# Performance work log

Hardware: AMD Instinct MI355X
Metric: run time of the kernel (lower is better)

Reference implementation:

```python
import jax, jax.numpy as jnp
import numpy as np

N_DIM = 32
N_HEADS = 4
HEAD_SIZE = N_DIM // N_HEADS  # 8


def setup_inputs() -> dict:
    key = jax.random.key(0)
    ks = jax.random.split(key, 9)
    B, T = 16, 2048
    s = 1.0 / np.sqrt(N_DIM)
    inp = {
        "x": jax.random.normal(ks[0], (B, T, N_DIM), dtype=jnp.float32),
        "Wq": jax.random.uniform(ks[1], (N_DIM, N_DIM), jnp.float32, -s, s),
        "bq": jax.random.uniform(ks[2], (N_DIM,), jnp.float32, -s, s),
        "Wk": jax.random.uniform(ks[3], (N_DIM, N_DIM), jnp.float32, -s, s),
        "bk": jax.random.uniform(ks[4], (N_DIM,), jnp.float32, -s, s),
        "Wv": jax.random.uniform(ks[5], (N_DIM, N_DIM), jnp.float32, -s, s),
        "bv": jax.random.uniform(ks[6], (N_DIM,), jnp.float32, -s, s),
        "Wp": jax.random.uniform(ks[7], (N_DIM, N_DIM), jnp.float32, -s, s),
        "bp": jax.random.uniform(ks[8], (N_DIM,), jnp.float32, -s, s),
    }
    return inp


def reference(x, Wq, bq, Wk, bk, Wv, bv, Wp, bp):
    b, t, c = x.shape
    # nn.Linear: y = x @ W^T + b
    def heads(W, bias):
        y = jnp.einsum("btc,dc->btd", x, W) + bias
        return y.reshape(b, t, N_HEADS, HEAD_SIZE).transpose(0, 2, 1, 3)  # [b,h,t,d]

    q = heads(Wq, bq)
    k = heads(Wk, bk)
    v = heads(Wv, bv)

    scores = jnp.einsum("bhqd,bhkd->bhqk", q, k) / np.sqrt(HEAD_SIZE)  # [b,h,t,t]
    causal = jnp.tril(jnp.ones((t, t), dtype=bool))
    scores = jnp.where(causal[None, None], scores, -jnp.inf)
    weights = jax.nn.softmax(scores, axis=-1)
    # dropout layers are identity in eval mode
    z = jnp.einsum("bhqk,bhkd->bhqd", weights, v)
    z = z.transpose(0, 2, 1, 3).reshape(b, t, N_DIM)
    z = jnp.einsum("btc,dc->btd", z, Wp) + bp
    return z
```

## Files before the change

### kernel.cpp

```cpp
#include <hip/hip_runtime.h>
#include <math.h>

#define BB 16
#define TT 2048
#define CC 32
#define HH 4
#define DD 8

#define KBS 2056
#define VRS 264
#define VBS (9 * VRS)
#define ZP 33

typedef __fp16 h2  __attribute__((ext_vector_type(2)));
typedef __fp16 h8  __attribute__((ext_vector_type(8)));
typedef float  fx16 __attribute__((ext_vector_type(16)));
typedef int    i4v __attribute__((ext_vector_type(4)));

__device__ __forceinline__ h2 pkh(float a, float b) {
#if __has_builtin(__builtin_amdgcn_cvt_pkrtz)
    return __builtin_amdgcn_cvt_pkrtz(a, b);
#else
    h2 r; r.x = (__fp16)a; r.y = (__fp16)b; return r;
#endif
}

__device__ __forceinline__ float fexp2(float x) {
#if __has_builtin(__builtin_amdgcn_exp2f)
    return __builtin_amdgcn_exp2f(x);
#else
    return exp2f(x);
#endif
}

__device__ __forceinline__ int h2bits(h2 v) { return __builtin_bit_cast(int, v); }

__device__ __forceinline__ void makeP(const fx16& S, bool last, int thr, int hi, h8* P) {
    float pe[16];
    #pragma unroll
    for (int r = 0; r < 16; r++) {
        const int ko = (r & 3) + 8 * (r >> 2);
        float sv = S[r];
        if (last) sv = (ko <= thr) ? sv : -INFINITY;
        pe[r] = fexp2(sv);
    }
    int Hh[8];
    #pragma unroll
    for (int i = 0; i < 8; i++) Hh[i] = h2bits(pkh(pe[2*i], pe[2*i+1]));
    #pragma unroll
    for (int s = 0; s < 2; s++) {
        const int b0 = 4 * s;
        int own0 = hi ? Hh[b0+2] : Hh[b0+0];
        int own1 = hi ? Hh[b0+3] : Hh[b0+1];
        int snd0 = hi ? Hh[b0+0] : Hh[b0+2];
        int snd1 = hi ? Hh[b0+1] : Hh[b0+3];
        int rcv0 = __shfl_xor(snd0, 32);
        int rcv1 = __shfl_xor(snd1, 32);
        i4v f;
        f.x = hi ? rcv0 : own0;
        f.y = hi ? rcv1 : own1;
        f.z = hi ? own0 : rcv0;
        f.w = hi ? own1 : rcv1;
        P[s] = __builtin_bit_cast(h8, f);
    }
}

__global__ __launch_bounds__(256) void qkv_kernel(
    const float* __restrict__ x,
    const float* __restrict__ Wq, const float* __restrict__ bq,
    const float* __restrict__ Wk, const float* __restrict__ bk,
    const float* __restrict__ Wv, const float* __restrict__ bv,
    __fp16* __restrict__ Qo, __fp16* __restrict__ Ko, __fp16* __restrict__ Vo)
{
    __shared__ float Xs[256 * ZP];
    const int tid = threadIdx.x;
    const int m = blockIdx.y >> 2, h = blockIdx.y & 3;
    const int row0 = blockIdx.x * 256;

    {
        const float4* xg = (const float4*)(x + (size_t)row0 * CC);
        #pragma unroll
        for (int i = 0; i < 8; i++) {
            const int idx = tid + 256 * i;
            float4 f = xg[idx];
            const int w = idx * 4;
            float* d = &Xs[(w >> 5) * ZP + (w & 31)];
            d[0] = f.x; d[1] = f.y; d[2] = f.z; d[3] = f.w;
        }
    }
    __syncthreads();

    const int row = row0 + tid;
    const int b = row >> 11, t = row & 2047;
    const int bh = b * HH + h;

    float xr[CC];
    #pragma unroll
    for (int c = 0; c < CC; c++) xr[c] = Xs[tid * ZP + c];

    const float* W    = (m == 0) ? Wq : (m == 1) ? Wk : Wv;
    const float* bias = (m == 0) ? bq : (m == 1) ? bk : bv;

    float o[DD];
    #pragma unroll
    for (int d = 0; d < DD; d++) {
        const int dd = h * DD + d;
        float acc = bias[dd];
        #pragma unroll
        for (int c = 0; c < CC; c++) acc += xr[c] * W[dd * CC + c];
        o[d] = acc;
    }

    if (m == 0) {
        const float qs = 0.3535533905932738f * 1.4426950408889634f;
        i4v qw;
        qw.x = h2bits(pkh(o[0]*qs, o[1]*qs)); qw.y = h2bits(pkh(o[2]*qs, o[3]*qs));
        qw.z = h2bits(pkh(o[4]*qs, o[5]*qs)); qw.w = h2bits(pkh(o[6]*qs, o[7]*qs));
        *(i4v*)(Qo + ((size_t)bh * TT + t) * DD) = qw;
    } else if (m == 1) {
        i4v kw;
        kw.x = h2bits(pkh(o[0], o[1])); kw.y = h2bits(pkh(o[2], o[3]));
        kw.z = h2bits(pkh(o[4], o[5])); kw.w = h2bits(pkh(o[6], o[7]));
        *(i4v*)(Ko + ((size_t)bh * TT + t) * DD) = kw;
    } else {
        __fp16* vt = Vo + (size_t)bh * 9 * TT + t;
        #pragma unroll
        for (int d = 0; d < DD; d++) vt[d * TT] = (__fp16)o[d];
        vt[8 * TT] = (__fp16)1.0f;
    }
}

__global__ __launch_bounds__(256, 2) void attn_kernel(
    const __fp16* __restrict__ Qg, const __fp16* __restrict__ Kg,
    const __fp16* __restrict__ Vg,
    const float* __restrict__ Wp, const float* __restrict__ bp,
    float* __restrict__ out)
{
    __shared__ __align__(16) __fp16 KsS[4 * KBS];
    __shared__ __align__(16) __fp16 VtS[4 * VBS];
    __shared__ float zbuf[64 * ZP];

    const int tid  = threadIdx.x;
    const int b    = blockIdx.x & 15;
    const int ip   = blockIdx.x >> 4;
    const int h    = tid >> 6;
    const int lane = tid & 63;
    const int qc   = lane & 31;
    const int hi   = lane >> 5;

    const int bh  = b * HH + h;
    const int qb1 = 32 * ip;
    const int qb2 = 32 * (63 - ip);
    const int keys_needed = qb2 + 32;
    const int nst = (keys_needed + 255) >> 8;

    h8 qf1, qf2;
    {
        h8 qz;
        #pragma unroll
        for (int i = 0; i < 8; i++) qz[i] = (__fp16)0.0f;
        h8 qa = *(const h8*)(Qg + ((size_t)bh * TT + qb1 + qc) * DD);
        h8 qb = *(const h8*)(Qg + ((size_t)bh * TT + qb2 + qc) * DD);
        qf1 = hi ? qz : qa;
        qf2 = hi ? qz : qb;
    }

    fx16 O1, O2, zc;
    #pragma unroll
    for (int i = 0; i < 16; i++) { O1[i] = 0.0f; O2[i] = 0.0f; zc[i] = 0.0f; }

    const int vrow = (qc < 9) ? qc : 8;
    const int thr  = qc - 4 * hi;

    const __fp16* kgl = Kg + (size_t)bh * TT * DD;
    const __fp16* vgl = Vg + (size_t)bh * 9 * TT;
    __fp16* kld = KsS + h * KBS;
    __fp16* vld = VtS + h * VBS;
    const __fp16* kb = kld + qc * DD;
    const __fp16* vb = vld + vrow * VRS + 8 * hi;

    i4v kpre[4], vpre[5];
    {
        const i4v* ks = (const i4v*)kgl;
        #pragma unroll
        for (int r = 0; r < 4; r++) kpre[r] = ks[lane + 64 * r];
        #pragma unroll
        for (int r = 0; r < 5; r++) {
            int i = lane + 64 * r; if (i > 287) i = 287;
            vpre[r] = *(const i4v*)(vgl + (i >> 5) * TT + (i & 31) * 8);
        }
    }

    for (int sti = 0; sti < nst; sti++) {
        const int st = sti * 256;
        {
            i4v* kd = (i4v*)kld;
            #pragma unroll
            for (int r = 0; r < 4; r++) kd[lane + 64 * r] = kpre[r];
            #pragma unroll
            for (int r = 0; r < 5; r++) {
                const int i = lane + 64 * r;
                if (i < 288) *(i4v*)(vld + (i >> 5) * VRS + (i & 31) * 8) = vpre[r];
            }
        }
        if (sti + 1 < nst) {
            const int st2 = st + 256;
            const i4v* ks = (const i4v*)(kgl + (size_t)st2 * DD);
            #pragma unroll
            for (int r = 0; r < 4; r++) kpre[r] = ks[lane + 64 * r];
            #pragma unroll
            for (int r = 0; r < 5; r++) {
                int i = lane + 64 * r; if (i > 287) i = 287;
                vpre[r] = *(const i4v*)(vgl + (i >> 5) * TT + st2 + (i & 31) * 8);
            }
        }

        const int kend = min(st + 256, keys_needed);
        for (int kt = st; kt < kend; kt += 32) {
            const bool a1 = (kt <= qb1);
            h8 kf = *(const h8*)(kb + (kt - st) * DD);

            h8 P1[2], P2[2];
            if (a1) {
                fx16 S = __builtin_amdgcn_mfma_f32_32x32x16_f16(kf, qf1, zc, 0, 0, 0);
                makeP(S, kt == qb1, thr, hi, P1);
            }
            {
                fx16 S = __builtin_amdgcn_mfma_f32_32x32x16_f16(kf, qf2, zc, 0, 0, 0);
                makeP(S, kt == qb2, thr, hi, P2);
            }
            #pragma unroll
            for (int s = 0; s < 2; s++) {
                h8 vf = *(const h8*)(vb + (kt - st) + 16 * s);
                if (a1) O1 = __builtin_amdgcn_mfma_f32_32x32x16_f16(vf, P1[s], O1, 0, 0, 0);
                O2 = __builtin_amdgcn_mfma_f32_32x32x16_f16(vf, P2[s], O2, 0, 0, 0);
            }
        }
    }

    {
        const float i1 = 1.0f / O1[4], i2 = 1.0f / O2[4];
        float* z1 = &zbuf[qc * ZP + h * DD + 4 * hi];
        float* z2 = &zbuf[(32 + qc) * ZP + h * DD + 4 * hi];
        z1[0] = O1[0]*i1; z1[1] = O1[1]*i1; z1[2] = O1[2]*i1; z1[3] = O1[3]*i1;
        z2[0] = O2[0]*i2; z2[1] = O2[1]*i2; z2[2] = O2[2]*i2; z2[3] = O2[3]*i2;
    }
    __syncthreads();

    {
        const int seg = tid >> 6;
        const int r = tid & 63;
        float zr[CC];
        #pragma unroll
        for (int c = 0; c < CC; c++) zr[c] = zbuf[r * ZP + c];
        float o[DD];
        #pragma unroll
        for (int d = 0; d < DD; d++) {
            const int dd = seg * DD + d;
            float acc = bp[dd];
            #pragma unroll
            for (int c = 0; c < CC; c++) acc += zr[c] * Wp[dd * CC + c];
            o[d] = acc;
        }
        const int qglob = (r < 32) ? (ip * 32 + r) : ((63 - ip) * 32 + (r - 32));
        float* dst = out + ((size_t)b * TT + qglob) * CC + seg * DD;
        ((float4*)dst)[0] = make_float4(o[0], o[1], o[2], o[3]);
        ((float4*)dst)[1] = make_float4(o[4], o[5], o[6], o[7]);
    }
}

extern "C" void kernel_launch(void* const* d_in, const int* in_sizes, int n_in,
                              void* d_out, int out_size, void* d_ws, size_t ws_size,
                              hipStream_t stream) {
    const float* x  = (const float*)d_in[0];
    const float* Wq = (const float*)d_in[1];
    const float* bq = (const float*)d_in[2];
    const float* Wk = (const float*)d_in[3];
    const float* bk = (const float*)d_in[4];
    const float* Wv = (const float*)d_in[5];
    const float* bv = (const float*)d_in[6];
    const float* Wp = (const float*)d_in[7];
    const float* bp = (const float*)d_in[8];
    float* out = (float*)d_out;

    const size_t NE = (size_t)BB * HH * TT * DD;
    __fp16* Qh = (__fp16*)d_ws;
    __fp16* Kh = Qh + NE;
    __fp16* Vt = Kh + NE;

    qkv_kernel<<<dim3(BB * TT / 256, 12), 256, 0, stream>>>(x, Wq, bq, Wk, bk, Wv, bv, Qh, Kh, Vt);
    attn_kernel<<<dim3(BB * 32), 256, 0, stream>>>(Qh, Kh, Vt, Wp, bp, out);
}
```

Before: 113.4 us.

## Split attention key range across two waves per head and merge partial outputs

The attention kernel now runs 8 waves per block, two per head. The causal key range of the paired query tiles is split between them so each wave does roughly balanced MFMA work. The partial unnormalized outputs (including the ones-row denominator) are summed through shared memory before normalization, and the output projection is spread over 8 waves. Separately, the QKV kernel computes all four heads per block instead of one, so each x tile is staged once per matrix rather than four times. The cost is more LDS per block, extra barriers and a reduction step.

New measurement: 137.5 us. +21.2%, slower.

```diff
diff --git a/kernel.cpp b/kernel.cpp
--- a/kernel.cpp
+++ b/kernel.cpp
@@ -74,7 +74,7 @@
 {
     __shared__ float Xs[256 * ZP];
     const int tid = threadIdx.x;
-    const int m = blockIdx.y >> 2, h = blockIdx.y & 3;
+    const int m = blockIdx.y;
     const int row0 = blockIdx.x * 256;
 
     {
@@ -92,7 +92,6 @@
 
     const int row = row0 + tid;
     const int b = row >> 11, t = row & 2047;
-    const int bh = b * HH + h;
 
     float xr[CC];
     #pragma unroll
@@ -101,58 +100,66 @@
     const float* W    = (m == 0) ? Wq : (m == 1) ? Wk : Wv;
     const float* bias = (m == 0) ? bq : (m == 1) ? bk : bv;
 
-    float o[DD];
-    #pragma unroll
-    for (int d = 0; d < DD; d++) {
-        const int dd = h * DD + d;
-        float acc = bias[dd];
-        #pragma unroll
-        for (int c = 0; c < CC; c++) acc += xr[c] * W[dd * CC + c];
-        o[d] = acc;
-    }
-
-    if (m == 0) {
-        const float qs = 0.3535533905932738f * 1.4426950408889634f;
-        i4v qw;
-        qw.x = h2bits(pkh(o[0]*qs, o[1]*qs)); qw.y = h2bits(pkh(o[2]*qs, o[3]*qs));
-        qw.z = h2bits(pkh(o[4]*qs, o[5]*qs)); qw.w = h2bits(pkh(o[6]*qs, o[7]*qs));
-        *(i4v*)(Qo + ((size_t)bh * TT + t) * DD) = qw;
-    } else if (m == 1) {
-        i4v kw;
-        kw.x = h2bits(pkh(o[0], o[1])); kw.y = h2bits(pkh(o[2], o[3]));
-        kw.z = h2bits(pkh(o[4], o[5])); kw.w = h2bits(pkh(o[6], o[7]));
-        *(i4v*)(Ko + ((size_t)bh * TT + t) * DD) = kw;
-    } else {
-        __fp16* vt = Vo + (size_t)bh * 9 * TT + t;
-        #pragma unroll
-        for (int d = 0; d < DD; d++) vt[d * TT] = (__fp16)o[d];
-        vt[8 * TT] = (__fp16)1.0f;
-    }
-}
-
-__global__ __launch_bounds__(256, 2) void attn_kernel(
+    for (int h = 0; h < HH; h++) {
+        const int bh = b * HH + h;
+        float o[DD];
+        #pragma unroll
+        for (int d = 0; d < DD; d++) {
+            const int dd = h * DD + d;
+            float acc = bias[dd];
+            #pragma unroll
+            for (int c = 0; c < CC; c++) acc += xr[c] * W[dd * CC + c];
+            o[d] = acc;
+        }
+        if (m == 0) {
+            const float qs = 0.3535533905932738f * 1.4426950408889634f;
+            i4v qw;
+            qw.x = h2bits(pkh(o[0]*qs, o[1]*qs)); qw.y = h2bits(pkh(o[2]*qs, o[3]*qs));
+            qw.z = h2bits(pkh(o[4]*qs, o[5]*qs)); qw.w = h2bits(pkh(o[6]*qs, o[7]*qs));
+            *(i4v*)(Qo + ((size_t)bh * TT + t) * DD) = qw;
+        } else if (m == 1) {
+            i4v kw;
+            kw.x = h2bits(pkh(o[0], o[1])); kw.y = h2bits(pkh(o[2], o[3]));
+            kw.z = h2bits(pkh(o[4], o[5])); kw.w = h2bits(pkh(o[6], o[7]));
+            *(i4v*)(Ko + ((size_t)bh * TT + t) * DD) = kw;
+        } else {
+            __fp16* vt = Vo + (size_t)bh * 9 * TT + t;
+            #pragma unroll
+            for (int d = 0; d < DD; d++) vt[d * TT] = (__fp16)o[d];
+            vt[8 * TT] = (__fp16)1.0f;
+        }
+    }
+}
+
+__global__ __launch_bounds__(512, 4) void attn_kernel(
     const __fp16* __restrict__ Qg, const __fp16* __restrict__ Kg,
     const __fp16* __restrict__ Vg,
     const float* __restrict__ Wp, const float* __restrict__ bp,
     float* __restrict__ out)
 {
-    __shared__ __align__(16) __fp16 KsS[4 * KBS];
-    __shared__ __align__(16) __fp16 VtS[4 * VBS];
+    __shared__ __align__(16) __fp16 KsS[8 * KBS];
+    __shared__ __align__(16) __fp16 VtS[8 * VBS];
     __shared__ float zbuf[64 * ZP];
 
-    const int tid  = threadIdx.x;
-    const int b    = blockIdx.x & 15;
-    const int ip   = blockIdx.x >> 4;
-    const int h    = tid >> 6;
-    const int lane = tid & 63;
-    const int qc   = lane & 31;
-    const int hi   = lane >> 5;
+    const int tid   = threadIdx.x;
+    const int b     = blockIdx.x & 15;
+    const int ip    = blockIdx.x >> 4;
+    const int wavei = tid >> 6;
+    const int h     = wavei >> 1;
+    const int half  = wavei & 1;
+    const int lane  = tid & 63;
+    const int qc    = lane & 31;
+    const int hi    = lane >> 5;
 
     const int bh  = b * HH + h;
+    const int T1  = ip + 1;
+    const int sA  = (63 - 2 * ip) >> 1;
     const int qb1 = 32 * ip;
     const int qb2 = 32 * (63 - ip);
-    const int keys_needed = qb2 + 32;
-    const int nst = (keys_needed + 255) >> 8;
+
+    const int ktLo = half ? 32 * sA : 0;
+    const int ktHi = half ? 32 * (64 - ip) : 32 * max(T1, sA);
+    const int g2lo = 32 * sA;
 
     h8 qf1, qf2;
     {
@@ -174,25 +181,26 @@
 
     const __fp16* kgl = Kg + (size_t)bh * TT * DD;
     const __fp16* vgl = Vg + (size_t)bh * 9 * TT;
-    __fp16* kld = KsS + h * KBS;
-    __fp16* vld = VtS + h * VBS;
+    __fp16* kld = KsS + wavei * KBS;
+    __fp16* vld = VtS + wavei * VBS;
     const __fp16* kb = kld + qc * DD;
     const __fp16* vb = vld + vrow * VRS + 8 * hi;
 
+    const int stLo = ktLo & ~255;
+
     i4v kpre[4], vpre[5];
     {
-        const i4v* ks = (const i4v*)kgl;
+        const i4v* ks = (const i4v*)(kgl + (size_t)stLo * DD);
         #pragma unroll
         for (int r = 0; r < 4; r++) kpre[r] = ks[lane + 64 * r];
         #pragma unroll
         for (int r = 0; r < 5; r++) {
             int i = lane + 64 * r; if (i > 287) i = 287;
-            vpre[r] = *(const i4v*)(vgl + (i >> 5) * TT + (i & 31) * 8);
-        }
-    }
-
-    for (int sti = 0; sti < nst; sti++) {
-        const int st = sti * 256;
+            vpre[r] = *(const i4v*)(vgl + (i >> 5) * TT + stLo + (i & 31) * 8);
+        }
+    }
+
+    for (int st = stLo; st < ktHi; st += 256) {
         {
             i4v* kd = (i4v*)kld;
             #pragma unroll
@@ -203,7 +211,7 @@
                 if (i < 288) *(i4v*)(vld + (i >> 5) * VRS + (i & 31) * 8) = vpre[r];
             }
         }
-        if (sti + 1 < nst) {
+        if (st + 256 < ktHi) {
             const int st2 = st + 256;
             const i4v* ks = (const i4v*)(kgl + (size_t)st2 * DD);
             #pragma unroll
@@ -215,9 +223,12 @@
             }
         }
 
-        const int kend = min(st + 256, keys_needed);
-        for (int kt = st; kt < kend; kt += 32) {
-            const bool a1 = (kt <= qb1);
+        const int k0 = max(st, ktLo);
+        const int k1 = min(st + 256, ktHi);
+        for (int kt = k0; kt < k1; kt += 32) {
+            const bool a1 = (half == 0) && (kt <= qb1);
+            const bool a2 = half ? true : (kt < g2lo);
+
             h8 kf = *(const h8*)(kb + (kt - st) * DD);
 
             h8 P1[2], P2[2];
@@ -225,7 +236,7 @@
                 fx16 S = __builtin_amdgcn_mfma_f32_32x32x16_f16(kf, qf1, zc, 0, 0, 0);
                 makeP(S, kt == qb1, thr, hi, P1);
             }
-            {
+            if (a2) {
                 fx16 S = __builtin_amdgcn_mfma_f32_32x32x16_f16(kf, qf2, zc, 0, 0, 0);
                 makeP(S, kt == qb2, thr, hi, P2);
             }
@@ -233,39 +244,50 @@
             for (int s = 0; s < 2; s++) {
                 h8 vf = *(const h8*)(vb + (kt - st) + 16 * s);
                 if (a1) O1 = __builtin_amdgcn_mfma_f32_32x32x16_f16(vf, P1[s], O1, 0, 0, 0);
-                O2 = __builtin_amdgcn_mfma_f32_32x32x16_f16(vf, P2[s], O2, 0, 0, 0);
-            }
-        }
-    }
+                if (a2) O2 = __builtin_amdgcn_mfma_f32_32x32x16_f16(vf, P2[s], O2, 0, 0, 0);
+            }
+        }
+    }
+
+    __syncthreads();
+    float* mb = (float*)(KsS + (size_t)(2 * h) * KBS);
+    if (half == 0) {
+        #pragma unroll
+        for (int r = 0; r < 16; r++) mb[r * 64 + lane] = O2[r];
+    }
+    __syncthreads();
+
+    if (half == 0) {
+        const float i1 = 1.0f / O1[4];
+        float* z1 = &zbuf[qc * ZP + h * DD + 4 * hi];
+        z1[0] = O1[0]*i1; z1[1] = O1[1]*i1; z1[2] = O1[2]*i1; z1[3] = O1[3]*i1;
+    } else {
+        #pragma unroll
+        for (int r = 0; r < 16; r++) O2[r] += mb[r * 64 + lane];
+        const float i2 = 1.0f / O2[4];
+        float* z2 = &zbuf[(32 + qc) * ZP + h * DD + 4 * hi];
+        z2[0] = O2[0]*i2; z2[1] = O2[1]*i2; z2[2] = O2[2]*i2; z2[3] = O2[3]*i2;
+    }
+    __syncthreads();
 
     {
-        const float i1 = 1.0f / O1[4], i2 = 1.0f / O2[4];
-        float* z1 = &zbuf[qc * ZP + h * DD + 4 * hi];
-        float* z2 = &zbuf[(32 + qc) * ZP + h * DD + 4 * hi];
-        z1[0] = O1[0]*i1; z1[1] = O1[1]*i1; z1[2] = O1[2]*i1; z1[3] = O1[3]*i1;
-        z2[0] = O2[0]*i2; z2[1] = O2[1]*i2; z2[2] = O2[2]*i2; z2[3] = O2[3]*i2;
-    }
-    __syncthreads();
-
-    {
-        const int seg = tid >> 6;
-        const int r = tid & 63;
+        const int seg = wavei;
+        const int r = lane;
         float zr[CC];
         #pragma unroll
         for (int c = 0; c < CC; c++) zr[c] = zbuf[r * ZP + c];
-        float o[DD];
-        #pragma unroll
-        for (int d = 0; d < DD; d++) {
-            const int dd = seg * DD + d;
+        float o4[4];
+        #pragma unroll
+        for (int d = 0; d < 4; d++) {
+            const int dd = seg * 4 + d;
             float acc = bp[dd];
             #pragma unroll
             for (int c = 0; c < CC; c++) acc += zr[c] * Wp[dd * CC + c];
-            o[d] = acc;
-        }
-        const int qglob = (r < 32) ? (ip * 32 + r) : ((63 - ip) * 32 + (r - 32));
-        float* dst = out + ((size_t)b * TT + qglob) * CC + seg * DD;
-        ((float4*)dst)[0] = make_float4(o[0], o[1], o[2], o[3]);
-        ((float4*)dst)[1] = make_float4(o[4], o[5], o[6], o[7]);
+            o4[d] = acc;
+        }
+        const int qglob = (r < 32) ? (qb1 + r) : (qb2 + (r - 32));
+        float* dst = out + ((size_t)b * TT + qglob) * CC + seg * 4;
+        *(float4*)dst = make_float4(o4[0], o4[1], o4[2], o4[3]);
     }
 }
 
@@ -288,6 +310,6 @@
     __fp16* Kh = Qh + NE;
     __fp16* Vt = Kh + NE;
 
-    qkv_kernel<<<dim3(BB * TT / 256, 12), 256, 0, stream>>>(x, Wq, bq, Wk, bk, Wv, bv, Qh, Kh, Vt);
-    attn_kernel<<<dim3(BB * 32), 256, 0, stream>>>(Qh, Kh, Vt, Wp, bp, out);
-}
+    qkv_kernel<<<dim3(BB * TT / 256, 3), 256, 0, stream>>>(x, Wq, bq, Wk, bk, Wv, bv, Qh, Kh, Vt);
+    attn_kernel<<<dim3(BB * 32), 512, 0, stream>>>(Qh, Kh, Vt, Wp, bp, out);
+}
```
